# Kernel optimization log

Hardware: AMD Instinct MI355X
Metric: run time of the kernel (lower is better)

## Reference

```python
import jax, jax.numpy as jnp
import numpy as np

DIM = 2048
NH = 16
HD = DIM // NH  # 128


def setup_inputs() -> dict:
    key = jax.random.key(0)
    ks = jax.random.split(key, 9)
    s_in = 1.0 / np.sqrt(DIM)
    inp = {
        "x": jax.random.normal(ks[0], (2, 2048, DIM), dtype=jnp.float32),
        # torch Linear weights stored as (out, in); we keep (in, out) for x @ W
        "wq": jax.random.uniform(ks[1], (DIM, DIM), jnp.float32, -s_in, s_in),
        "bq": jax.random.uniform(ks[2], (DIM,), jnp.float32, -s_in, s_in),
        "wk": jax.random.uniform(ks[3], (DIM, HD), jnp.float32, -s_in, s_in),
        "bk": jax.random.uniform(ks[4], (HD,), jnp.float32, -s_in, s_in),
        "wv": jax.random.uniform(ks[5], (DIM, HD), jnp.float32, -s_in, s_in),
        "bv": jax.random.uniform(ks[6], (HD,), jnp.float32, -s_in, s_in),
        "wo": jax.random.uniform(ks[7], (DIM, DIM), jnp.float32, -s_in, s_in),
        "bo": jax.random.uniform(ks[8], (DIM,), jnp.float32, -s_in, s_in),
    }
    return inp


def reference(x, wq, bq, wk, bk, wv, bv, wo, bo):
    bs, sl, dim = x.shape
    q = x @ wq + bq                      # [b, s, dim]
    k = x @ wk + bk                      # [b, s, hd] (single shared KV head)
    v = x @ wv + bv                      # [b, s, hd]
    q = q.reshape(bs, sl, NH, HD)        # [b, s, h, hd]
    scale = 1.0 / np.sqrt(HD).astype(np.float32)
    # scores: broadcast single KV head over all query heads
    attn = jnp.einsum('bshd,btd->bhst', q, k) * scale   # [b, h, s, s]
    att = jax.nn.softmax(attn, axis=-1)
    o = jnp.einsum('bhst,btd->bshd', att, v)            # [b, s, h, hd]
    o = o.reshape(bs, sl, dim)
    return o @ wo + bo
```

## Files before the change

kernel.cpp:

```cpp
#include <hip/hip_runtime.h>
#include <hip/hip_bf16.h>
#include <math.h>

#define DIM 2048
#define NH 16
#define HD 128
#define BATCH 2
#define SEQ 2048
#define TOKENS (BATCH * SEQ)
#define NQKV (DIM + 2 * HD)

typedef __attribute__((ext_vector_type(8))) _Float16 f16x8;
typedef __attribute__((ext_vector_type(2))) _Float16 f16x2;
typedef __attribute__((ext_vector_type(4))) float f32x4;
typedef unsigned short u16;
typedef unsigned int u32;

typedef union { u32 d[4]; f16x8 v; } frag_u;

__device__ __forceinline__ u16 f2h(float f) {
    union { _Float16 h; u16 u; } v; v.h = (_Float16)f; return v.u;
}
__device__ __forceinline__ void gll16(const void* g, void* l) {
    __builtin_amdgcn_global_load_lds(
        (const __attribute__((address_space(1))) unsigned int*)g,
        (__attribute__((address_space(3))) unsigned int*)l, 16, 0, 0);
}

#define KIDX(r, c) ((r) * 128 + (((((c) << 1)) ^ (((r) & 7) << 4)) >> 1))
#define VIDX(d, c) ((d) * 64  + (((((c) << 1)) ^ (((d) & 7) << 4)) >> 1))

__global__ __launch_bounds__(256) void conv_f16(
    const float* __restrict__ in, u16* __restrict__ out)
{
    const int i = blockIdx.x * 256 + threadIdx.x;
    const float4 v = ((const float4*)in)[i];
    ushort4 h;
    h.x = f2h(v.x); h.y = f2h(v.y); h.z = f2h(v.z); h.w = f2h(v.w);
    ((ushort4*)out)[i] = h;
}

__global__ __launch_bounds__(256) void transpose_f16(
    const float* __restrict__ W, u16* __restrict__ T, int K, int N, int rowoff)
{
    __shared__ float tile[32][33];
    const int k0 = blockIdx.x * 32;
    const int n0 = blockIdx.y * 32;
    const int tid = threadIdx.x;
#pragma unroll
    for (int i = 0; i < 4; ++i) {
        const int idx = tid + i * 256;
        const int r = idx >> 5, c = idx & 31;
        tile[r][c] = W[(size_t)(k0 + r) * N + n0 + c];
    }
    __syncthreads();
#pragma unroll
    for (int i = 0; i < 4; ++i) {
        const int idx = tid + i * 256;
        const int r = idx >> 5, c = idx & 31;
        T[(size_t)(rowoff + n0 + r) * K + k0 + c] = f2h(tile[c][r]);
    }
}

__global__ __launch_bounds__(256) void concat_bias(
    const float* __restrict__ bq, const float* __restrict__ bk,
    const float* __restrict__ bv, float* __restrict__ bc)
{
    const int i = blockIdx.x * 256 + threadIdx.x;
    float v;
    if (i < DIM) v = bq[i];
    else if (i < DIM + HD) v = bk[i - DIM];
    else v = bv[i - DIM - HD];
    bc[i] = v;
}

template <int MODE>
__global__ __launch_bounds__(256) void gemm_f16(
    const u16* __restrict__ A, const u16* __restrict__ B,
    const float* __restrict__ bias, float* __restrict__ Cf,
    u16* __restrict__ qdst, u16* __restrict__ kdst, u16* __restrict__ vtdst,
    float scale)
{
    constexpr int BK = 32;
    __shared__ u16 lds[2][2 * 128 * BK];

    const int tid = threadIdx.x;
    const int wid = tid >> 6;
    const int lane = tid & 63;
    const int lr = lane & 15;
    const int lhi = lane >> 4;
    const int wr = wid >> 1, wc = wid & 1;
    const int bm = blockIdx.y * 128;
    const int bn = blockIdx.x * 128;

    f32x4 acc[4][4];
#pragma unroll
    for (int i = 0; i < 4; ++i)
#pragma unroll
        for (int j = 0; j < 4; ++j) acc[i][j] = (f32x4){0.f, 0.f, 0.f, 0.f};

#define STAGE(buf_, k0_)                                                      \
    {                                                                         \
        _Pragma("unroll")                                                     \
        for (int rr = 0; rr < 2; ++rr) {                                      \
            const int slot = rr * 256 + tid;                                  \
            const int row = slot >> 2;                                        \
            const int gch = ((slot & 3) ^ ((row >> 1) & 3)) * 8;              \
            char* lbase = (char*)lds[buf_] + (size_t)(rr * 256 + wid * 64) * 16; \
            gll16(A + (size_t)(bm + row) * DIM + (k0_) + gch, lbase);         \
            gll16(B + (size_t)(bn + row) * DIM + (k0_) + gch, lbase + 8192);  \
        }                                                                     \
    }

    STAGE(0, 0);
    __syncthreads();

    int cur = 0;
    for (int k0 = 0; k0 < DIM; k0 += BK) {
        if (k0 + BK < DIM) STAGE(cur ^ 1, k0 + BK);

        f16x8 a[4], b[4];
#pragma unroll
        for (int i = 0; i < 4; ++i) {
            const int mrow = wr * 64 + i * 16 + lr;
            const int nrow = wc * 64 + i * 16 + lr;
            a[i] = *(const f16x8*)&lds[cur][mrow * BK + ((lhi ^ ((mrow >> 1) & 3)) * 8)];
            b[i] = *(const f16x8*)&lds[cur][4096 + nrow * BK + ((lhi ^ ((nrow >> 1) & 3)) * 8)];
        }
        __builtin_amdgcn_s_setprio(1);
#pragma unroll
        for (int i = 0; i < 4; ++i)
#pragma unroll
            for (int j = 0; j < 4; ++j)
                acc[i][j] = __builtin_amdgcn_mfma_f32_16x16x32_f16(a[i], b[j], acc[i][j], 0, 0, 0);
        __builtin_amdgcn_s_setprio(0);
        __syncthreads();
        cur ^= 1;
    }
#undef STAGE

    const float alpha = (MODE == 0 && bn < DIM) ? scale : 1.0f;
    float bj[4];
#pragma unroll
    for (int j = 0; j < 4; ++j) bj[j] = bias[bn + wc * 64 + j * 16 + lr];

#pragma unroll
    for (int i = 0; i < 4; ++i) {
#pragma unroll
        for (int j = 0; j < 4; ++j) {
#pragma unroll
            for (int r = 0; r < 4; ++r) {
                const int row = bm + wr * 64 + i * 16 + lhi * 4 + r;
                const int col = bn + wc * 64 + j * 16 + lr;
                const float val = (acc[i][j][r] + bj[j]) * alpha;
                if (MODE == 1) {
                    Cf[(size_t)row * DIM + col] = val;
                } else if (bn < DIM) {
                    qdst[(size_t)row * DIM + col] = f2h(val);
                } else if (bn < DIM + HD) {
                    kdst[(size_t)row * HD + (col - DIM)] = f2h(val);
                } else {
                    vtdst[(size_t)(col - DIM - HD) * TOKENS + row] = f2h(val);
                }
            }
        }
    }
}

__global__ __launch_bounds__(256, 2) void mqa_attn_f16(
    const u16* __restrict__ Q, const u16* __restrict__ Kg,
    const u16* __restrict__ Vtg, u16* __restrict__ Oh)
{
    __shared__ __align__(16) u16 Ks[2][64 * 128];
    __shared__ __align__(16) u16 Vt[2][128 * 64];

    const int tid = threadIdx.x;
    const int wid = tid >> 6;
    const int lane = tid & 63;
    const int lr = lane & 15;
    const int lhi = lane >> 4;
    const bool l5 = (lhi & 2) != 0;

    const int qt = blockIdx.x;
    const int h  = blockIdx.y;
    const int b  = blockIdx.z;
    const size_t bseq = (size_t)b * SEQ;
    const int q0 = qt * 128 + wid * 32;

    f16x8 qf[2][4];
#pragma unroll
    for (int mt = 0; mt < 2; ++mt) {
        const u16* qrow = Q + (bseq + q0 + mt * 16 + lr) * DIM + (size_t)h * HD;
#pragma unroll
        for (int kk = 0; kk < 4; ++kk)
            qf[mt][kk] = *(const f16x8*)(qrow + kk * 32 + lhi * 8);
    }

    f16x8 ones;
#pragma unroll
    for (int j = 0; j < 8; ++j) ones[j] = (_Float16)1.0f;

    f32x4 o[2][8];
#pragma unroll
    for (int mt = 0; mt < 2; ++mt)
#pragma unroll
        for (int dt = 0; dt < 8; ++dt) o[mt][dt] = (f32x4){0.f, 0.f, 0.f, 0.f};
    float m[2]    = {-INFINITY, -INFINITY};
    float lsum[2] = {0.f, 0.f};

#define STAGE_KV(buf_, t0_)                                                   \
    {                                                                         \
        _Pragma("unroll")                                                     \
        for (int i = 0; i < 4; ++i) {                                         \
            const int L = i * 256 + tid;                                      \
            char* kbase = (char*)&Ks[buf_][0] + (size_t)(i * 256 + wid * 64) * 16; \
            char* vbase = (char*)&Vt[buf_][0] + (size_t)(i * 256 + wid * 64) * 16; \
            const int krow = L >> 4, kc = (L & 15) ^ ((L >> 4) & 7);          \
            const int vrow = L >> 3, vc = (L & 7) ^ ((L >> 3) & 7);           \
            gll16(&Kg[(bseq + (t0_) + krow) * HD + kc * 8], kbase);           \
            gll16(&Vtg[(size_t)vrow * TOKENS + bseq + (t0_) + vc * 8], vbase);\
        }                                                                     \
    }

    STAGE_KV(0, 0);
    __syncthreads();

    int cur = 0;
    for (int t0 = 0; t0 < SEQ; t0 += 64) {
        if (t0 + 64 < SEQ) STAGE_KV(cur ^ 1, t0 + 64);

        f32x4 sc[2][4];
#pragma unroll
        for (int mt = 0; mt < 2; ++mt)
#pragma unroll
            for (int ct = 0; ct < 4; ++ct) sc[mt][ct] = (f32x4){0.f, 0.f, 0.f, 0.f};
        __builtin_amdgcn_s_setprio(1);
#pragma unroll
        for (int kk = 0; kk < 4; ++kk)
#pragma unroll
            for (int ct = 0; ct < 4; ++ct) {
                const f16x8 kf = *(const f16x8*)&Ks[cur][KIDX(ct * 16 + lr, kk * 32 + lhi * 8)];
                sc[0][ct] = __builtin_amdgcn_mfma_f32_16x16x32_f16(kf, qf[0][kk], sc[0][ct], 0, 0, 0);
                sc[1][ct] = __builtin_amdgcn_mfma_f32_16x16x32_f16(kf, qf[1][kk], sc[1][ct], 0, 0, 0);
            }
        __builtin_amdgcn_s_setprio(0);

        frag_u pa[2][2];
        float al[2];
#pragma unroll
        for (int mt = 0; mt < 2; ++mt) {
            float pm = fmaxf(fmaxf(fmaxf(sc[mt][0][0], sc[mt][0][1]),
                                   fmaxf(sc[mt][0][2], sc[mt][0][3])),
                             fmaxf(fmaxf(sc[mt][1][0], sc[mt][1][1]),
                                   fmaxf(sc[mt][1][2], sc[mt][1][3])));
            pm = fmaxf(pm, fmaxf(fmaxf(fmaxf(sc[mt][2][0], sc[mt][2][1]),
                                       fmaxf(sc[mt][2][2], sc[mt][2][3])),
                                 fmaxf(fmaxf(sc[mt][3][0], sc[mt][3][1]),
                                       fmaxf(sc[mt][3][2], sc[mt][3][3]))));
            pm = fmaxf(pm, __shfl_xor(pm, 16));
            pm = fmaxf(pm, __shfl_xor(pm, 32));

            const bool grow = pm > m[mt] + 8.f;
            al[mt] = 1.f;
            if (__any(grow)) {
                if (grow) { al[mt] = __expf(m[mt] - pm); m[mt] = pm; }
#pragma unroll
                for (int dt = 0; dt < 8; ++dt)
#pragma unroll
                    for (int r = 0; r < 4; ++r)
                        o[mt][dt][r] *= al[mt];
            }

            u32 pk[4][2];
#pragma unroll
            for (int ct = 0; ct < 4; ++ct) {
                const float p0 = __expf(sc[mt][ct][0] - m[mt]);
                const float p1 = __expf(sc[mt][ct][1] - m[mt]);
                const float p2 = __expf(sc[mt][ct][2] - m[mt]);
                const float p3 = __expf(sc[mt][ct][3] - m[mt]);
                pk[ct][0] = __builtin_bit_cast(u32, __builtin_amdgcn_cvt_pkrtz(p0, p1));
                pk[ct][1] = __builtin_bit_cast(u32, __builtin_amdgcn_cvt_pkrtz(p2, p3));
            }

#pragma unroll
            for (int kk = 0; kk < 2; ++kk)
#pragma unroll
                for (int p = 0; p < 2; ++p) {
                    const u32 X = pk[2 * kk + 0][p];
                    const u32 Y = pk[2 * kk + 1][p];
                    const u32 sx = __shfl_xor(X, 32);
                    const u32 sy = __shfl_xor(Y, 32);
                    const u32 X1 = l5 ? sy : X;
                    const u32 Y1 = l5 ? Y : sx;
                    const auto u2 = __builtin_amdgcn_permlane16_swap(X1, Y1, false, false);
                    pa[mt][kk].d[p]     = u2[0];
                    pa[mt][kk].d[2 + p] = u2[1];
                }
        }

        f32x4 lacc[2];
        lacc[0] = (f32x4){0.f, 0.f, 0.f, 0.f};
        lacc[1] = (f32x4){0.f, 0.f, 0.f, 0.f};
        __builtin_amdgcn_s_setprio(1);
#pragma unroll
        for (int kk = 0; kk < 2; ++kk) {
            lacc[0] = __builtin_amdgcn_mfma_f32_16x16x32_f16(ones, pa[0][kk].v, lacc[0], 0, 0, 0);
            lacc[1] = __builtin_amdgcn_mfma_f32_16x16x32_f16(ones, pa[1][kk].v, lacc[1], 0, 0, 0);
#pragma unroll
            for (int dt = 0; dt < 8; ++dt) {
                const f16x8 vf = *(const f16x8*)&Vt[cur][VIDX(dt * 16 + lr, kk * 32 + lhi * 8)];
                o[0][dt] = __builtin_amdgcn_mfma_f32_16x16x32_f16(vf, pa[0][kk].v, o[0][dt], 0, 0, 0);
                o[1][dt] = __builtin_amdgcn_mfma_f32_16x16x32_f16(vf, pa[1][kk].v, o[1][dt], 0, 0, 0);
            }
        }
        __builtin_amdgcn_s_setprio(0);
#pragma unroll
        for (int mt = 0; mt < 2; ++mt)
            lsum[mt] = lsum[mt] * al[mt] + lacc[mt][0];

        __syncthreads();
        cur ^= 1;
    }
#undef STAGE_KV

#pragma unroll
    for (int mt = 0; mt < 2; ++mt) {
        const float inv = 1.f / lsum[mt];
        const size_t base = (bseq + q0 + mt * 16 + lr) * DIM + (size_t)h * HD + lhi * 4;
#pragma unroll
        for (int dt = 0; dt < 8; ++dt) {
            ushort4 h4;
            h4.x = f2h(o[mt][dt][0] * inv);
            h4.y = f2h(o[mt][dt][1] * inv);
            h4.z = f2h(o[mt][dt][2] * inv);
            h4.w = f2h(o[mt][dt][3] * inv);
            *(ushort4*)&Oh[base + dt * 16] = h4;
        }
    }
}

extern "C" void kernel_launch(void* const* d_in, const int* in_sizes, int n_in,
                              void* d_out, int out_size, void* d_ws, size_t ws_size,
                              hipStream_t stream) {
    const float* x  = (const float*)d_in[0];
    const float* wq = (const float*)d_in[1];
    const float* bq = (const float*)d_in[2];
    const float* wk = (const float*)d_in[3];
    const float* bk = (const float*)d_in[4];
    const float* wv = (const float*)d_in[5];
    const float* bv = (const float*)d_in[6];
    const float* wo = (const float*)d_in[7];
    const float* bo = (const float*)d_in[8];
    float* out = (float*)d_out;

    char* w = (char*)d_ws;
    u16* xh     = (u16*)w;                 w += (size_t)TOKENS * DIM * 2;
    u16* wcat   = (u16*)w;                 w += (size_t)NQKV * DIM * 2;
    u16* woT    = (u16*)w;                 w += (size_t)DIM * DIM * 2;
    u16* qb     = (u16*)w;                 w += (size_t)TOKENS * DIM * 2;
    u16* kb     = (u16*)w;                 w += (size_t)TOKENS * HD * 2;
    u16* vtb    = (u16*)w;                 w += (size_t)TOKENS * HD * 2;
    float* bc   = (float*)w;               w += 16384;
    u16* Oh = xh;

    const float scale = 0.08838834764831845f;
    const dim3 blk(256);

    conv_f16<<<TOKENS * DIM / 4 / 256, blk, 0, stream>>>(x, xh);
    transpose_f16<<<dim3(DIM / 32, DIM / 32), blk, 0, stream>>>(wq, wcat, DIM, DIM, 0);
    transpose_f16<<<dim3(DIM / 32, HD / 32), blk, 0, stream>>>(wk, wcat, DIM, HD, DIM);
    transpose_f16<<<dim3(DIM / 32, HD / 32), blk, 0, stream>>>(wv, wcat, DIM, HD, DIM + HD);
    transpose_f16<<<dim3(DIM / 32, DIM / 32), blk, 0, stream>>>(wo, woT, DIM, DIM, 0);
    concat_bias<<<NQKV / 256, blk, 0, stream>>>(bq, bk, bv, bc);

    gemm_f16<0><<<dim3(NQKV / 128, TOKENS / 128), blk, 0, stream>>>(
        xh, wcat, bc, nullptr, qb, kb, vtb, scale);

    mqa_attn_f16<<<dim3(SEQ / 128, NH, BATCH), blk, 0, stream>>>(qb, kb, vtb, Oh);

    gemm_f16<1><<<dim3(DIM / 128, TOKENS / 128), blk, 0, stream>>>(
        Oh, woT, bo, out, nullptr, nullptr, nullptr, 1.0f);
}
```

Before: 224.6 us.

## Read K/V fragments directly from global memory instead of LDS double buffer

Removes the LDS double-buffered K/V staging and the per-tile block barrier in the attention kernel. Each wave now loads its K and V^T MFMA fragments straight from global memory, relying on L1/L2 caching because the single shared KV head is reused by every query head and tile. The online-softmax rescale is also reordered so the output and running-sum scaling happen after the P computation. The change drops LDS traffic and synchronisation but exposes global-load latency with no software prefetch, and each wave re-reads the same K/V data.

Result: slower. 399.8 us (+78.0%).

```diff
diff --git a/kernel.cpp b/kernel.cpp
--- a/kernel.cpp
+++ b/kernel.cpp
@@ -11,7 +11,6 @@
 #define NQKV (DIM + 2 * HD)
 
 typedef __attribute__((ext_vector_type(8))) _Float16 f16x8;
-typedef __attribute__((ext_vector_type(2))) _Float16 f16x2;
 typedef __attribute__((ext_vector_type(4))) float f32x4;
 typedef unsigned short u16;
 typedef unsigned int u32;
@@ -26,9 +25,6 @@
         (const __attribute__((address_space(1))) unsigned int*)g,
         (__attribute__((address_space(3))) unsigned int*)l, 16, 0, 0);
 }
-
-#define KIDX(r, c) ((r) * 128 + (((((c) << 1)) ^ (((r) & 7) << 4)) >> 1))
-#define VIDX(d, c) ((d) * 64  + (((((c) << 1)) ^ (((d) & 7) << 4)) >> 1))
 
 __global__ __launch_bounds__(256) void conv_f16(
     const float* __restrict__ in, u16* __restrict__ out)
@@ -171,9 +167,6 @@
     const u16* __restrict__ Q, const u16* __restrict__ Kg,
     const u16* __restrict__ Vtg, u16* __restrict__ Oh)
 {
-    __shared__ __align__(16) u16 Ks[2][64 * 128];
-    __shared__ __align__(16) u16 Vt[2][128 * 64];
-
     const int tid = threadIdx.x;
     const int wid = tid >> 6;
     const int lane = tid & 63;
@@ -208,27 +201,10 @@
     float m[2]    = {-INFINITY, -INFINITY};
     float lsum[2] = {0.f, 0.f};
 
-#define STAGE_KV(buf_, t0_)                                                   \
-    {                                                                         \
-        _Pragma("unroll")                                                     \
-        for (int i = 0; i < 4; ++i) {                                         \
-            const int L = i * 256 + tid;                                      \
-            char* kbase = (char*)&Ks[buf_][0] + (size_t)(i * 256 + wid * 64) * 16; \
-            char* vbase = (char*)&Vt[buf_][0] + (size_t)(i * 256 + wid * 64) * 16; \
-            const int krow = L >> 4, kc = (L & 15) ^ ((L >> 4) & 7);          \
-            const int vrow = L >> 3, vc = (L & 7) ^ ((L >> 3) & 7);           \
-            gll16(&Kg[(bseq + (t0_) + krow) * HD + kc * 8], kbase);           \
-            gll16(&Vtg[(size_t)vrow * TOKENS + bseq + (t0_) + vc * 8], vbase);\
-        }                                                                     \
-    }
-
-    STAGE_KV(0, 0);
-    __syncthreads();
-
-    int cur = 0;
+    const u16* kp = Kg + (bseq + lr) * HD + lhi * 8;
+    const u16* vp = Vtg + (size_t)lr * TOKENS + bseq + lhi * 8;
+
     for (int t0 = 0; t0 < SEQ; t0 += 64) {
-        if (t0 + 64 < SEQ) STAGE_KV(cur ^ 1, t0 + 64);
-
         f32x4 sc[2][4];
 #pragma unroll
         for (int mt = 0; mt < 2; ++mt)
@@ -239,7 +215,8 @@
         for (int kk = 0; kk < 4; ++kk)
 #pragma unroll
             for (int ct = 0; ct < 4; ++ct) {
-                const f16x8 kf = *(const f16x8*)&Ks[cur][KIDX(ct * 16 + lr, kk * 32 + lhi * 8)];
+                const f16x8 kf =
+                    *(const f16x8*)(kp + (size_t)(t0 + ct * 16) * HD + kk * 32);
                 sc[0][ct] = __builtin_amdgcn_mfma_f32_16x16x32_f16(kf, qf[0][kk], sc[0][ct], 0, 0, 0);
                 sc[1][ct] = __builtin_amdgcn_mfma_f32_16x16x32_f16(kf, qf[1][kk], sc[1][ct], 0, 0, 0);
             }
@@ -261,27 +238,21 @@
             pm = fmaxf(pm, __shfl_xor(pm, 32));
 
             const bool grow = pm > m[mt] + 8.f;
-            al[mt] = 1.f;
-            if (__any(grow)) {
-                if (grow) { al[mt] = __expf(m[mt] - pm); m[mt] = pm; }
-#pragma unroll
-                for (int dt = 0; dt < 8; ++dt)
-#pragma unroll
-                    for (int r = 0; r < 4; ++r)
-                        o[mt][dt][r] *= al[mt];
-            }
+            const float mnew = grow ? pm : m[mt];
+            al[mt] = grow ? __expf(m[mt] - mnew) : 1.f;
+            const bool anyg = __any(grow);
+            m[mt] = mnew;
 
             u32 pk[4][2];
 #pragma unroll
             for (int ct = 0; ct < 4; ++ct) {
-                const float p0 = __expf(sc[mt][ct][0] - m[mt]);
-                const float p1 = __expf(sc[mt][ct][1] - m[mt]);
-                const float p2 = __expf(sc[mt][ct][2] - m[mt]);
-                const float p3 = __expf(sc[mt][ct][3] - m[mt]);
+                const float p0 = __expf(sc[mt][ct][0] - mnew);
+                const float p1 = __expf(sc[mt][ct][1] - mnew);
+                const float p2 = __expf(sc[mt][ct][2] - mnew);
+                const float p3 = __expf(sc[mt][ct][3] - mnew);
                 pk[ct][0] = __builtin_bit_cast(u32, __builtin_amdgcn_cvt_pkrtz(p0, p1));
                 pk[ct][1] = __builtin_bit_cast(u32, __builtin_amdgcn_cvt_pkrtz(p2, p3));
             }
-
 #pragma unroll
             for (int kk = 0; kk < 2; ++kk)
 #pragma unroll
@@ -296,6 +267,15 @@
                     pa[mt][kk].d[p]     = u2[0];
                     pa[mt][kk].d[2 + p] = u2[1];
                 }
+
+            if (anyg) {
+#pragma unroll
+                for (int dt = 0; dt < 8; ++dt)
+#pragma unroll
+                    for (int r = 0; r < 4; ++r)
+                        o[mt][dt][r] *= al[mt];
+                lsum[mt] *= al[mt];
+            }
         }
 
         f32x4 lacc[2];
@@ -308,20 +288,16 @@
             lacc[1] = __builtin_amdgcn_mfma_f32_16x16x32_f16(ones, pa[1][kk].v, lacc[1], 0, 0, 0);
 #pragma unroll
             for (int dt = 0; dt < 8; ++dt) {
-                const f16x8 vf = *(const f16x8*)&Vt[cur][VIDX(dt * 16 + lr, kk * 32 + lhi * 8)];
+                const f16x8 vf =
+                    *(const f16x8*)(vp + (size_t)(dt * 16) * TOKENS + t0 + kk * 32);
                 o[0][dt] = __builtin_amdgcn_mfma_f32_16x16x32_f16(vf, pa[0][kk].v, o[0][dt], 0, 0, 0);
                 o[1][dt] = __builtin_amdgcn_mfma_f32_16x16x32_f16(vf, pa[1][kk].v, o[1][dt], 0, 0, 0);
             }
         }
         __builtin_amdgcn_s_setprio(0);
-#pragma unroll
-        for (int mt = 0; mt < 2; ++mt)
-            lsum[mt] = lsum[mt] * al[mt] + lacc[mt][0];
-
-        __syncthreads();
-        cur ^= 1;
-    }
-#undef STAGE_KV
+        lsum[0] += lacc[0][0];
+        lsum[1] += lacc[1][0];
+    }
 
 #pragma unroll
     for (int mt = 0; mt < 2; ++mt) {
```
